# Optimization experiments

Hardware: AMD Instinct MI355X
Metric: run time of the kernel (lower is better)

The kernel has to match this reference:

```python
import jax, jax.numpy as jnp
import numpy as np
import math

V, P, D, L, H = 50257, 1024, 768, 12, 12
HD = D // H
DFF = 4 * D
B, S = 2, 1024
EPS = 1e-5


def setup_inputs() -> dict:
    key = jax.random.key(0)
    ks = jax.random.split(key, 8)
    sc = 0.02
    return {
        "input_ids": jax.random.randint(ks[0], (B, S), 0, V),
        "wte": jax.random.normal(ks[1], (V, D), jnp.float32) * sc,
        "wpe": jax.random.normal(ks[2], (P, D), jnp.float32) * sc,
        "ln1_g": jnp.ones((L, D), jnp.float32),
        "ln1_b": jnp.zeros((L, D), jnp.float32),
        "qkv_w": jax.random.normal(ks[3], (L, 3 * D, D), jnp.float32) * sc,
        "qkv_b": jnp.zeros((L, 3 * D), jnp.float32),
        "proj_w": jax.random.normal(ks[4], (L, D, D), jnp.float32) * sc,
        "proj_b": jnp.zeros((L, D), jnp.float32),
        "ln2_g": jnp.ones((L, D), jnp.float32),
        "ln2_b": jnp.zeros((L, D), jnp.float32),
        "fc_w": jax.random.normal(ks[5], (L, DFF, D), jnp.float32) * sc,
        "fc_b": jnp.zeros((L, DFF), jnp.float32),
        "cproj_w": jax.random.normal(ks[6], (L, D, DFF), jnp.float32) * sc,
        "cproj_b": jnp.zeros((L, D), jnp.float32),
        "lnf_g": jnp.ones((D,), jnp.float32),
        "lnf_b": jnp.zeros((D,), jnp.float32),
    }


def layer_norm(x, g, b):
    mu = jnp.mean(x, axis=-1, keepdims=True)
    var = jnp.mean(jnp.square(x - mu), axis=-1, keepdims=True)
    return (x - mu) * jax.lax.rsqrt(var + EPS) * g + b


def _forward(input_ids, wte, wpe, ln1_g, ln1_b, qkv_w, qkv_b, proj_w, proj_b,
             ln2_g, ln2_b, fc_w, fc_b, cproj_w, cproj_b, lnf_g, lnf_b):
    s = input_ids.shape[1]
    h = wte[input_ids] + wpe[jnp.arange(s)][None, :, :]  # [B,S,D]
    causal = jnp.tril(jnp.ones((s, s), bool))  # [S,S]
    neg_inf = jnp.finfo(h.dtype).min

    def step(x, p):
        l1g, l1b, qw, qb, pw, pb, l2g, l2b, fw, fb, cw, cb = p
        hn = layer_norm(x, l1g, l1b)
        qkv = hn @ qw.T + qb  # [B,S,3D]
        q, k, v = jnp.split(qkv, 3, axis=-1)
        q = q.reshape(B, s, H, HD).transpose(0, 2, 1, 3)  # [B,H,S,hd]
        k = k.reshape(B, s, H, HD).transpose(0, 2, 1, 3)
        v = v.reshape(B, s, H, HD).transpose(0, 2, 1, 3)
        scores = jnp.einsum("bhqd,bhkd->bhqk", q, k) / math.sqrt(HD)
        scores = jnp.where(causal[None, None], scores, neg_inf)
        attn = jax.nn.softmax(scores, axis=-1)
        o = jnp.einsum("bhqk,bhkd->bhqd", attn, v)
        o = o.transpose(0, 2, 1, 3).reshape(B, s, D)
        x = x + (o @ pw.T + pb)
        hn2 = layer_norm(x, l2g, l2b)
        m = jax.nn.gelu(hn2 @ fw.T + fb, approximate=False)
        x = x + (m @ cw.T + cb)
        return x, None

    params = (ln1_g, ln1_b, qkv_w, qkv_b, proj_w, proj_b,
              ln2_g, ln2_b, fc_w, fc_b, cproj_w, cproj_b)
    h, _ = jax.lax.scan(step, h, params)
    h = layer_norm(h, lnf_g, lnf_b)
    logits = h @ wte.T  # tied lm_head, [B,S,V]
    return logits


def reference(input_ids, wte, wpe, ln1_g, ln1_b, qkv_w, qkv_b, proj_w, proj_b,
              ln2_g, ln2_b, fc_w, fc_b, cproj_w, cproj_b, lnf_g, lnf_b):
    return _forward(input_ids, wte, wpe, ln1_g, ln1_b, qkv_w, qkv_b, proj_w,
                    proj_b, ln2_g, ln2_b, fc_w, fc_b, cproj_w, cproj_b,
                    lnf_g, lnf_b)
```

## Files before the change

kernel.cpp:

```cpp
#include <hip/hip_runtime.h>

#define BB 2
#define SS 1024
#define DM 768
#define NH 12
#define HDIM 64
#define NL 12
#define DFFN 3072
#define VOC 50257
#define ROWS (BB * SS)
#define MT (ROWS / 128)

typedef __attribute__((ext_vector_type(4))) float f32x4;
typedef __attribute__((ext_vector_type(8))) short short8;
typedef __attribute__((ext_vector_type(4))) short short4v;
typedef unsigned short ushort;

__device__ __forceinline__ ushort f2bf(float f) {
  union { float f; unsigned int u; } x; x.f = f;
  unsigned int u = x.u;
  unsigned int r = (u + 0x7FFFu + ((u >> 16) & 1u)) >> 16;
  return (ushort)r;
}

__global__ __launch_bounds__(256) void embed_k(const int* __restrict__ ids,
    const float* __restrict__ wte, const float* __restrict__ wpe,
    float* __restrict__ h) {
  const int row = blockIdx.x;
  const int s = row & (SS - 1);
  const int tid = threadIdx.x;
  const int id = ids[row];
  const size_t wbase = (size_t)id * DM;
  const size_t pbase = (size_t)s * DM;
  const size_t obase = (size_t)row * DM;
  h[obase + tid]       = wte[wbase + tid]       + wpe[pbase + tid];
  h[obase + tid + 256] = wte[wbase + tid + 256] + wpe[pbase + tid + 256];
  h[obase + tid + 512] = wte[wbase + tid + 512] + wpe[pbase + tid + 512];
}

__global__ __launch_bounds__(256) void f2b_k(const float* __restrict__ in,
                                             ushort* __restrict__ out, int n4) {
  for (int i = blockIdx.x * 256 + threadIdx.x; i < n4; i += gridDim.x * 256) {
    f32x4 v = ((const f32x4*)in)[i];
    short4v s;
    s[0] = f2bf(v[0]); s[1] = f2bf(v[1]); s[2] = f2bf(v[2]); s[3] = f2bf(v[3]);
    ((short4v*)out)[i] = s;
  }
}

template <int OB>
__global__ __launch_bounds__(256) void layernorm_t(const float* __restrict__ x,
    const float* __restrict__ g, const float* __restrict__ b, void* __restrict__ y) {
  const int tid = threadIdx.x;
  const int lane = tid & 63;
  const int wave = tid >> 6;
  const int row = blockIdx.x * 4 + wave;
  const size_t base = (size_t)row * DM;

  f32x4 v[3];
  float sum = 0.f;
#pragma unroll
  for (int k = 0; k < 3; k++) {
    v[k] = *(const f32x4*)&x[base + k * 256 + lane * 4];
    sum += v[k][0] + v[k][1] + v[k][2] + v[k][3];
  }
#pragma unroll
  for (int off = 32; off >= 1; off >>= 1) sum += __shfl_xor(sum, off);
  const float mu = sum * (1.0f / DM);

  float var = 0.f;
#pragma unroll
  for (int k = 0; k < 3; k++)
#pragma unroll
    for (int i = 0; i < 4; i++) {
      const float d = v[k][i] - mu;
      var += d * d;
    }
#pragma unroll
  for (int off = 32; off >= 1; off >>= 1) var += __shfl_xor(var, off);
  const float rstd = rsqrtf(var * (1.0f / DM) + 1e-5f);

#pragma unroll
  for (int k = 0; k < 3; k++) {
    const int col = k * 256 + lane * 4;
    f32x4 gv = *(const f32x4*)&g[col];
    f32x4 bv = *(const f32x4*)&b[col];
    if (OB) {
      short4v o;
#pragma unroll
      for (int i = 0; i < 4; i++)
        o[i] = f2bf((v[k][i] - mu) * rstd * gv[i] + bv[i]);
      *(short4v*)&((ushort*)y)[base + col] = o;
    } else {
      f32x4 o;
#pragma unroll
      for (int i = 0; i < 4; i++)
        o[i] = (v[k][i] - mu) * rstd * gv[i] + bv[i];
      *(f32x4*)&((float*)y)[base + col] = o;
    }
  }
}

template <int ROUNDS>
__device__ __forceinline__ void stage_sw(const ushort* __restrict__ g, int ldg,
                                         ushort* lds, int wave, int lane,
                                         int rowmax) {
#pragma unroll
  for (int r = 0; r < ROUNDS; r++) {
    const int chunk = (r * 4 + wave) * 64 + lane;
    const int nrow = chunk >> 3;
    const int cs = (chunk & 7) ^ (nrow & 7);
    const int row = nrow > rowmax ? rowmax : nrow;
    const ushort* ga = g + (size_t)row * ldg + cs * 8;
    ushort* la = lds + (r * 4 + wave) * 512;
    __builtin_amdgcn_global_load_lds(
        (const __attribute__((address_space(1))) unsigned int*)ga,
        (__attribute__((address_space(3))) unsigned int*)la, 16, 0, 0);
  }
}

__global__ __launch_bounds__(256) void gemm_lg(const ushort* __restrict__ A,
    const ushort* __restrict__ Bw, float* __restrict__ Cout, int N, int K) {
  __shared__ __align__(16) ushort smem[4 * 8192];
  ushort* AsL0 = smem;
  ushort* AsL1 = smem + 8192;
  ushort* BsL0 = smem + 16384;
  ushort* BsL1 = smem + 24576;

  const int tid = threadIdx.x;
  const int lane = tid & 63;
  const int wave = tid >> 6;
  const int la = lane & 15;
  const int hi = lane >> 4;
  const int swz = (la & 7) << 3;

  const int nwg = gridDim.x;
  int bid = blockIdx.x;
  {
    const int q = nwg >> 3, r = nwg & 7;
    const int xcd = bid & 7, idx = bid >> 3;
    bid = (xcd < r ? xcd * (q + 1) : r * (q + 1) + (xcd - r) * q) + idx;
  }
  const int m0 = (bid % MT) * 128;
  const int n0 = (bid / MT) * 128;

  const int wr = (wave >> 1) * 64;
  const int wc = (wave & 1) * 64;
  const int brmax = min(N - n0 - 1, 127);

  f32x4 acc[4][4];
#pragma unroll
  for (int i = 0; i < 4; i++)
#pragma unroll
    for (int j = 0; j < 4; j++) acc[i][j] = (f32x4){0.f, 0.f, 0.f, 0.f};

  const ushort* Ag = A + (size_t)m0 * K;
  const ushort* Bg = Bw + (size_t)n0 * K;

  const int nt = K >> 6;
  const int s0 = (bid % MT) % nt;

  stage_sw<4>(Ag + s0 * 64, K, AsL0, wave, lane, 127);
  stage_sw<4>(Bg + s0 * 64, K, BsL0, wave, lane, brmax);

  int cur = 0;
  for (int t = 0; t < nt; t++) {
    if (t + 1 < nt) {
      int sn = t + 1 + s0; if (sn >= nt) sn -= nt;
      stage_sw<4>(Ag + sn * 64, K, cur ? AsL0 : AsL1, wave, lane, 127);
      stage_sw<4>(Bg + sn * 64, K, cur ? BsL0 : BsL1, wave, lane, brmax);
      asm volatile("s_waitcnt vmcnt(8)" ::: "memory");
    } else {
      asm volatile("s_waitcnt vmcnt(0)" ::: "memory");
    }
    __builtin_amdgcn_s_barrier();
    __builtin_amdgcn_sched_barrier(0);

    const ushort* Ab = (cur ? AsL1 : AsL0) + (wr + la) * 64;
    const ushort* Bb = (cur ? BsL1 : BsL0) + (wc + la) * 64;
    __builtin_amdgcn_s_setprio(1);
#pragma unroll
    for (int ks = 0; ks < 2; ks++) {
      const int co = (ks * 32 + hi * 8) ^ swz;
      short8 a[4], b[4];
#pragma unroll
      for (int mi = 0; mi < 4; mi++)
        a[mi] = *(const short8*)(Ab + mi * 1024 + co);
#pragma unroll
      for (int ni = 0; ni < 4; ni++)
        b[ni] = *(const short8*)(Bb + ni * 1024 + co);
#pragma unroll
      for (int mi = 0; mi < 4; mi++)
#pragma unroll
        for (int ni = 0; ni < 4; ni++)
          acc[mi][ni] = __builtin_amdgcn_mfma_f32_16x16x32_bf16(
              a[mi], b[ni], acc[mi][ni], 0, 0, 0);
    }
    __builtin_amdgcn_s_setprio(0);
    __builtin_amdgcn_sched_barrier(0);
    __builtin_amdgcn_s_barrier();
    __builtin_amdgcn_sched_barrier(0);
    cur ^= 1;
  }

  float* L = (float*)smem;
  const int myhalf = wave & 1;
#pragma unroll
  for (int h = 0; h < 2; h++) {
    if (myhalf == h) {
#pragma unroll
      for (int mi = 0; mi < 4; mi++)
#pragma unroll
        for (int ni = 0; ni < 4; ni++)
#pragma unroll
          for (int j = 0; j < 4; j++) {
            const int row = wr + mi * 16 + 4 * hi + j;
            const int col = ni * 16 + la;
            L[row * 68 + col] = acc[mi][ni][j];
          }
    }
    __syncthreads();
#pragma unroll
    for (int it = 0; it < 32; it++) {
      const int flat = it * 256 + tid;
      const int row = flat >> 6, col = flat & 63;
      const int gc = n0 + h * 64 + col;
      if (gc < N)
        Cout[(size_t)(m0 + row) * N + gc] = L[row * 68 + col];
    }
    __syncthreads();
  }
}

template <int EPI, int OUTBF, int MR>
__global__ __launch_bounds__(256) void gemm_p3(const ushort* __restrict__ A,
    const ushort* __restrict__ Bw, const float* __restrict__ bias,
    const float* __restrict__ res, void* __restrict__ Cout, int N, int K) {
  constexpr int MROWS = MR * 32;
  constexpr int MTILES = ROWS / MROWS;
  constexpr int ASZ = MROWS * 64;
  constexpr int BSZ = 64 * 64;
  __shared__ __align__(16) ushort smem[3 * ASZ + 3 * BSZ];
  ushort* As = smem;
  ushort* Bs = smem + 3 * ASZ;

  const int tid = threadIdx.x;
  const int lane = tid & 63;
  const int wave = tid >> 6;
  const int la = lane & 15;
  const int hi = lane >> 4;
  const int swz = (la & 7) << 3;

  const int nwg = gridDim.x;
  int bid = blockIdx.x;
  {
    const int q = nwg >> 3, r = nwg & 7;
    const int xcd = bid & 7, idx = bid >> 3;
    bid = (xcd < r ? xcd * (q + 1) : r * (q + 1) + (xcd - r) * q) + idx;
  }
  const int m0 = (bid % MTILES) * MROWS;
  const int n0 = (bid / MTILES) * 64;

  const int wr = (wave >> 1) * (MROWS / 2);
  const int wc = (wave & 1) * 32;

  f32x4 acc[MR][2];
#pragma unroll
  for (int i = 0; i < MR; i++)
#pragma unroll
    for (int j = 0; j < 2; j++) acc[i][j] = (f32x4){0.f, 0.f, 0.f, 0.f};

  const ushort* Ag = A + (size_t)m0 * K;
  const ushort* Bg = Bw + (size_t)n0 * K;
  const int nt = K >> 6;
  const int s0 = (bid % MTILES) % nt;

  {
    int s1 = s0 + 1; if (s1 >= nt) s1 -= nt;
    stage_sw<MR>(Ag + s0 * 64, K, As, wave, lane, MROWS - 1);
    stage_sw<2>(Bg + s0 * 64, K, Bs, wave, lane, 63);
    stage_sw<MR>(Ag + s1 * 64, K, As + ASZ, wave, lane, MROWS - 1);
    stage_sw<2>(Bg + s1 * 64, K, Bs + BSZ, wave, lane, 63);
  }

  for (int t = 0; t < nt; t++) {
    if (t + 1 < nt) {
      asm volatile("s_waitcnt vmcnt(%0)" :: "i"(MR + 2) : "memory");
    } else {
      asm volatile("s_waitcnt vmcnt(0)" ::: "memory");
    }
    __builtin_amdgcn_s_barrier();
    __builtin_amdgcn_sched_barrier(0);

    const ushort* Ab = As + (t % 3) * ASZ + (wr + la) * 64;
    const ushort* Bb = Bs + (t % 3) * BSZ + (wc + la) * 64;
    __builtin_amdgcn_s_setprio(1);
#pragma unroll
    for (int ks = 0; ks < 2; ks++) {
      const int co = (ks * 32 + hi * 8) ^ swz;
      short8 a[MR], b[2];
#pragma unroll
      for (int mi = 0; mi < MR; mi++)
        a[mi] = *(const short8*)(Ab + mi * 1024 + co);
#pragma unroll
      for (int ni = 0; ni < 2; ni++)
        b[ni] = *(const short8*)(Bb + ni * 1024 + co);
#pragma unroll
      for (int mi = 0; mi < MR; mi++)
#pragma unroll
        for (int ni = 0; ni < 2; ni++)
          acc[mi][ni] = __builtin_amdgcn_mfma_f32_16x16x32_bf16(
              a[mi], b[ni], acc[mi][ni], 0, 0, 0);
    }
    __builtin_amdgcn_s_setprio(0);
    __builtin_amdgcn_sched_barrier(0);
    __builtin_amdgcn_s_barrier();
    __builtin_amdgcn_sched_barrier(0);
    if (t + 2 < nt) {
      int sn = t + 2 + s0; if (sn >= nt) sn -= nt;
      stage_sw<MR>(Ag + sn * 64, K, As + ((t + 2) % 3) * ASZ, wave, lane, MROWS - 1);
      stage_sw<2>(Bg + sn * 64, K, Bs + ((t + 2) % 3) * BSZ, wave, lane, 63);
    }
  }

  if (OUTBF) {
    ushort* L = smem;
#pragma unroll
    for (int mi = 0; mi < MR; mi++)
#pragma unroll
      for (int ni = 0; ni < 2; ni++)
#pragma unroll
        for (int j = 0; j < 4; j++) {
          const int row = wr + mi * 16 + 4 * hi + j;
          const int col = wc + ni * 16 + la;
          float x = acc[mi][ni][j];
          if (EPI >= 1) x += bias[n0 + col];
          if (EPI == 3) x = 0.5f * x * (1.0f + erff(x * 0.70710678118f));
          L[row * 72 + col] = f2bf(x);
        }
    __syncthreads();
    ushort* Co = (ushort*)Cout;
    constexpr int ITERS = MROWS * 64 / 8 / 256;
#pragma unroll
    for (int it = 0; it < ITERS; it++) {
      const int idx8 = it * 256 + tid;
      const int row = idx8 >> 3, c8 = idx8 & 7;
      short8 v = *(const short8*)&L[row * 72 + c8 * 8];
      *(short8*)&Co[(size_t)(m0 + row) * N + n0 + c8 * 8] = v;
    }
  } else {
    float* L = (float*)smem;
#pragma unroll
    for (int mi = 0; mi < MR; mi++)
#pragma unroll
      for (int ni = 0; ni < 2; ni++)
#pragma unroll
        for (int j = 0; j < 4; j++) {
          const int row = wr + mi * 16 + 4 * hi + j;
          const int col = wc + ni * 16 + la;
          float x = acc[mi][ni][j];
          if (EPI >= 1) x += bias[n0 + col];
          if (EPI == 3) x = 0.5f * x * (1.0f + erff(x * 0.70710678118f));
          L[row * 68 + col] = x;
        }
    __syncthreads();
    f32x4* Co = (f32x4*)Cout;
    const f32x4* R4 = (const f32x4*)res;
    constexpr int ITERS = MROWS * 64 / 4 / 256;
#pragma unroll
    for (int it = 0; it < ITERS; it++) {
      const int idx4 = it * 256 + tid;
      const int row = idx4 >> 4, c4 = idx4 & 15;
      f32x4 v = *(const f32x4*)&L[row * 68 + c4 * 4];
      const size_t o4 = ((size_t)(m0 + row) * N + n0) / 4 + c4;
      if (EPI == 2) v += R4[o4];
      Co[o4] = v;
    }
  }
}

__global__ __launch_bounds__(256) void attn_bf(const ushort* __restrict__ qkv,
                                               ushort* __restrict__ o) {
  const int tid = threadIdx.x;
  const int lane = tid & 63;
  const int wave = tid >> 6;
  const int hi = lane >> 4;
  const int la = lane & 15;
  const int q0 = blockIdx.x * 64;
  const int bh = blockIdx.y;
  const int bb = bh / NH;
  const int hh = bh % NH;
  const size_t rstride = 3 * DM;
  const ushort* base = qkv + (size_t)bb * SS * rstride;
  const ushort* kbase = base + DM + hh * HDIM;
  const ushort* vbase = base + 2 * DM + hh * HDIM;

  __shared__ ushort Ks[64][72];
  __shared__ ushort Vt[64][72];
  __shared__ ushort Pb[4][16][72];

  const int kr = tid >> 2;
  const int kc = (tid & 3) * 16;
  const int vp0 = (tid >> 3) * 2;
  const int vc = (tid & 7) * 8;

  short8 qf[2];
  {
    const int qrow = q0 + wave * 16 + la;
    const ushort* qp = base + (size_t)qrow * rstride + hh * HDIM + 8 * hi;
    qf[0] = *(const short8*)qp;
    qf[1] = *(const short8*)(qp + 32);
  }

  short8 kA, kB, vA, vB;
  {
    const ushort* kp = kbase + (size_t)kr * rstride + kc;
    kA = *(const short8*)kp;
    kB = *(const short8*)(kp + 8);
    const ushort* vp = vbase + (size_t)vp0 * rstride + vc;
    vA = *(const short8*)vp;
    vB = *(const short8*)(vp + rstride);
  }

  f32x4 accO[4] = {};
  float m_[4], l_[4];
#pragma unroll
  for (int j = 0; j < 4; j++) { m_[j] = -1e30f; l_[j] = 0.f; }

  const int nt = q0 / 64 + 1;
  for (int kt = 0; kt < nt; kt++) {
    __syncthreads();
    *(short8*)&Ks[kr][kc]     = kA;
    *(short8*)&Ks[kr][kc + 8] = kB;
#pragma unroll
    for (int i = 0; i < 8; i++) {
      unsigned int pk = (unsigned int)(unsigned short)vA[i] |
                        ((unsigned int)(unsigned short)vB[i] << 16);
      *(unsigned int*)&Vt[vc + i][vp0] = pk;
    }
    __syncthreads();
    if (kt + 1 < nt) {
      const ushort* kp = kbase + (size_t)((kt + 1) * 64 + kr) * rstride + kc;
      kA = *(const short8*)kp;
      kB = *(const short8*)(kp + 8);
      const ushort* vp = vbase + (size_t)((kt + 1) * 64 + vp0) * rstride + vc;
      vA = *(const short8*)vp;
      vB = *(const short8*)(vp + rstride);
    }

    f32x4 s[4] = {};
#pragma unroll
    for (int f = 0; f < 4; f++) {
#pragma unroll
      for (int kk = 0; kk < 2; kk++) {
        short8 kf = *(const short8*)&Ks[f * 16 + la][kk * 32 + 8 * hi];
        s[f] = __builtin_amdgcn_mfma_f32_16x16x32_bf16(qf[kk], kf, s[f], 0, 0, 0);
      }
#pragma unroll
      for (int j = 0; j < 4; j++) s[f][j] *= 0.125f;
    }

    if (kt == nt - 1) {
      const int qr = wave * 16 + 4 * hi;
#pragma unroll
      for (int f = 0; f < 4; f++) {
        const int kcol = f * 16 + la;
#pragma unroll
        for (int j = 0; j < 4; j++)
          if (kcol > qr + j) s[f][j] = -1e30f;
      }
    }

#pragma unroll
    for (int j = 0; j < 4; j++) {
      float rm = fmaxf(fmaxf(s[0][j], s[1][j]), fmaxf(s[2][j], s[3][j]));
      rm = fmaxf(rm, __shfl_xor(rm, 1));
      rm = fmaxf(rm, __shfl_xor(rm, 2));
      rm = fmaxf(rm, __shfl_xor(rm, 4));
      rm = fmaxf(rm, __shfl_xor(rm, 8));
      const float mnew = fmaxf(m_[j], rm);
      const float alpha = expf(m_[j] - mnew);
      float rs = 0.f;
#pragma unroll
      for (int f = 0; f < 4; f++) {
        const float p = expf(s[f][j] - mnew);
        s[f][j] = p;
        rs += p;
      }
      rs += __shfl_xor(rs, 1);
      rs += __shfl_xor(rs, 2);
      rs += __shfl_xor(rs, 4);
      rs += __shfl_xor(rs, 8);
      l_[j] = l_[j] * alpha + rs;
      m_[j] = mnew;
#pragma unroll
      for (int f = 0; f < 4; f++) accO[f][j] *= alpha;
    }

#pragma unroll
    for (int f = 0; f < 4; f++)
#pragma unroll
      for (int j = 0; j < 4; j++)
        Pb[wave][4 * hi + j][f * 16 + la] = f2bf(s[f][j]);

    short8 pf0 = *(const short8*)&Pb[wave][la][8 * hi];
    short8 pf1 = *(const short8*)&Pb[wave][la][32 + 8 * hi];
#pragma unroll
    for (int f = 0; f < 4; f++) {
      short8 vf0 = *(const short8*)&Vt[f * 16 + la][8 * hi];
      short8 vf1 = *(const short8*)&Vt[f * 16 + la][32 + 8 * hi];
      accO[f] = __builtin_amdgcn_mfma_f32_16x16x32_bf16(pf0, vf0, accO[f], 0, 0, 0);
      accO[f] = __builtin_amdgcn_mfma_f32_16x16x32_bf16(pf1, vf1, accO[f], 0, 0, 0);
    }
  }

  ushort* op = o + (size_t)(bb * SS + q0 + wave * 16) * DM + hh * HDIM;
#pragma unroll
  for (int j = 0; j < 4; j++) {
    const float inv = 1.0f / l_[j];
    const int qr = 4 * hi + j;
#pragma unroll
    for (int f = 0; f < 4; f++)
      op[(size_t)qr * DM + f * 16 + la] = f2bf(accO[f][j] * inv);
  }
}

template <int EPI>
__global__ __launch_bounds__(256) void gemm_nt(const float* __restrict__ A,
    const float* __restrict__ Bw, const float* __restrict__ bias,
    const float* __restrict__ res, float* __restrict__ C, int N, int K) {
  __shared__ ushort As[64][40];
  __shared__ ushort Bs[64][40];
  const int tid = threadIdx.x;
  const int m0 = blockIdx.y * 64;
  const int n0 = blockIdx.x * 64;
  const int lane = tid & 63;
  const int wave = tid >> 6;
  const int wr = (wave >> 1) * 32;
  const int wc = (wave & 1) * 32;
  const int lr = lane & 15;
  const int lk = (lane >> 4) * 8;
  const int sr = tid >> 2;
  const int sc = (tid & 3) * 8;
  f32x4 acc[2][2] = {};
  for (int kk = 0; kk < K; kk += 32) {
    {
      const float* p = A + (size_t)(m0 + sr) * K + kk + sc;
      f32x4 v0 = *(const f32x4*)p;
      f32x4 v1 = *(const f32x4*)(p + 4);
      short8 sv;
      for (int i = 0; i < 4; i++) { sv[i] = f2bf(v0[i]); sv[4 + i] = f2bf(v1[i]); }
      *(short8*)&As[sr][sc] = sv;
    }
    {
      const int gr = n0 + sr;
      short8 sv = {};
      if (gr < N) {
        const float* p = Bw + (size_t)gr * K + kk + sc;
        f32x4 v0 = *(const f32x4*)p;
        f32x4 v1 = *(const f32x4*)(p + 4);
        for (int i = 0; i < 4; i++) { sv[i] = f2bf(v0[i]); sv[4 + i] = f2bf(v1[i]); }
      }
      *(short8*)&Bs[sr][sc] = sv;
    }
    __syncthreads();
    short8 a0 = *(const short8*)&As[wr + lr][lk];
    short8 a1 = *(const short8*)&As[wr + 16 + lr][lk];
    short8 b0 = *(const short8*)&Bs[wc + lr][lk];
    short8 b1 = *(const short8*)&Bs[wc + 16 + lr][lk];
    acc[0][0] = __builtin_amdgcn_mfma_f32_16x16x32_bf16(a0, b0, acc[0][0], 0, 0, 0);
    acc[0][1] = __builtin_amdgcn_mfma_f32_16x16x32_bf16(a0, b1, acc[0][1], 0, 0, 0);
    acc[1][0] = __builtin_amdgcn_mfma_f32_16x16x32_bf16(a1, b0, acc[1][0], 0, 0, 0);
    acc[1][1] = __builtin_amdgcn_mfma_f32_16x16x32_bf16(a1, b1, acc[1][1], 0, 0, 0);
    __syncthreads();
  }
  const int orow = (lane >> 4) * 4;
  for (int mi = 0; mi < 2; mi++)
    for (int ni = 0; ni < 2; ni++) {
      const int col = n0 + wc + ni * 16 + lr;
      if (col >= N) continue;
      for (int j = 0; j < 4; j++) {
        const int row = m0 + wr + mi * 16 + orow + j;
        float x = acc[mi][ni][j];
        if (EPI >= 1) x += bias[col];
        const size_t idx = (size_t)row * N + col;
        if (EPI == 2) x += res[idx];
        if (EPI == 3) x = 0.5f * x * (1.0f + erff(x * 0.70710678118f));
        C[idx] = x;
      }
    }
}

__global__ __launch_bounds__(256) void attn_f32(const float* __restrict__ qkv,
                                                float* __restrict__ o) {
  const int tid = threadIdx.x;
  const int lane = tid & 63;
  const int wave = tid >> 6;
  const int hi = lane >> 4;
  const int la = lane & 15;
  const int q0 = blockIdx.x * 64;
  const int bh = blockIdx.y;
  const int bb = bh / NH;
  const int hh = bh % NH;
  const size_t rstride = 3 * DM;
  const float* base = qkv + (size_t)bb * SS * rstride;
  __shared__ ushort Ks[64][72];
  __shared__ ushort Vt[64][72];
  __shared__ ushort Pb[4][16][72];
  short8 qf[2];
  {
    const int qrow = q0 + wave * 16 + la;
    const float* qp = base + (size_t)qrow * rstride + hh * HDIM + 8 * hi;
    for (int kk = 0; kk < 2; kk++) {
      f32x4 v0 = *(const f32x4*)(qp + 32 * kk);
      f32x4 v1 = *(const f32x4*)(qp + 32 * kk + 4);
      short8 sv;
      for (int i = 0; i < 4; i++) {
        sv[i] = f2bf(v0[i] * 0.125f); sv[4 + i] = f2bf(v1[i] * 0.125f);
      }
      qf[kk] = sv;
    }
  }
  f32x4 accO[4] = {};
  float m_[4], l_[4];
  for (int j = 0; j < 4; j++) { m_[j] = -1e30f; l_[j] = 0.f; }
  const int nt = q0 / 64 + 1;
  for (int kt = 0; kt < nt; kt++) {
    __syncthreads();
    {
      const int r = tid >> 2;
      const int c = (tid & 3) * 16;
      const float* kp = base + (size_t)(kt * 64 + r) * rstride + DM + hh * HDIM + c;
      const float* vp = kp + DM;
      f32x4 k0 = *(const f32x4*)kp, k1 = *(const f32x4*)(kp + 4);
      f32x4 k2 = *(const f32x4*)(kp + 8), k3 = *(const f32x4*)(kp + 12);
      short8 s0, s1;
      for (int i = 0; i < 4; i++) {
        s0[i] = f2bf(k0[i]); s0[4 + i] = f2bf(k1[i]);
        s1[i] = f2bf(k2[i]); s1[4 + i] = f2bf(k3[i]);
      }
      *(short8*)&Ks[r][c] = s0;
      *(short8*)&Ks[r][c + 8] = s1;
      f32x4 v0 = *(const f32x4*)vp, v1 = *(const f32x4*)(vp + 4);
      f32x4 v2 = *(const f32x4*)(vp + 8), v3 = *(const f32x4*)(vp + 12);
      for (int i = 0; i < 4; i++) {
        Vt[c + i][r] = f2bf(v0[i]); Vt[c + 4 + i][r] = f2bf(v1[i]);
        Vt[c + 8 + i][r] = f2bf(v2[i]); Vt[c + 12 + i][r] = f2bf(v3[i]);
      }
    }
    __syncthreads();
    f32x4 s[4] = {};
    for (int f = 0; f < 4; f++)
      for (int kk = 0; kk < 2; kk++) {
        short8 kf = *(const short8*)&Ks[f * 16 + la][kk * 32 + 8 * hi];
        s[f] = __builtin_amdgcn_mfma_f32_16x16x32_bf16(qf[kk], kf, s[f], 0, 0, 0);
      }
    if (kt == nt - 1) {
      const int qr = wave * 16 + 4 * hi;
      for (int f = 0; f < 4; f++) {
        const int kcol = f * 16 + la;
        for (int j = 0; j < 4; j++)
          if (kcol > qr + j) s[f][j] = -1e30f;
      }
    }
    for (int j = 0; j < 4; j++) {
      float rm = fmaxf(fmaxf(s[0][j], s[1][j]), fmaxf(s[2][j], s[3][j]));
      rm = fmaxf(rm, __shfl_xor(rm, 1));
      rm = fmaxf(rm, __shfl_xor(rm, 2));
      rm = fmaxf(rm, __shfl_xor(rm, 4));
      rm = fmaxf(rm, __shfl_xor(rm, 8));
      const float mnew = fmaxf(m_[j], rm);
      const float alpha = expf(m_[j] - mnew);
      float rs = 0.f;
      for (int f = 0; f < 4; f++) {
        const float p = expf(s[f][j] - mnew);
        s[f][j] = p; rs += p;
      }
      rs += __shfl_xor(rs, 1);
      rs += __shfl_xor(rs, 2);
      rs += __shfl_xor(rs, 4);
      rs += __shfl_xor(rs, 8);
      l_[j] = l_[j] * alpha + rs;
      m_[j] = mnew;
      for (int f = 0; f < 4; f++) accO[f][j] *= alpha;
    }
    for (int f = 0; f < 4; f++)
      for (int j = 0; j < 4; j++)
        Pb[wave][4 * hi + j][f * 16 + la] = f2bf(s[f][j]);
    short8 pf0 = *(const short8*)&Pb[wave][la][8 * hi];
    short8 pf1 = *(const short8*)&Pb[wave][la][32 + 8 * hi];
    for (int f = 0; f < 4; f++) {
      short8 vf0 = *(const short8*)&Vt[f * 16 + la][8 * hi];
      short8 vf1 = *(const short8*)&Vt[f * 16 + la][32 + 8 * hi];
      accO[f] = __builtin_amdgcn_mfma_f32_16x16x32_bf16(pf0, vf0, accO[f], 0, 0, 0);
      accO[f] = __builtin_amdgcn_mfma_f32_16x16x32_bf16(pf1, vf1, accO[f], 0, 0, 0);
    }
  }
  float* op = o + (size_t)(bb * SS + q0 + wave * 16) * DM + hh * HDIM;
  for (int j = 0; j < 4; j++) {
    const float inv = 1.0f / l_[j];
    const int qr = 4 * hi + j;
    for (int f = 0; f < 4; f++)
      op[(size_t)qr * DM + f * 16 + la] = accO[f][j] * inv;
  }
}

extern "C" void kernel_launch(void* const* d_in, const int* in_sizes, int n_in,
                              void* d_out, int out_size, void* d_ws,
                              size_t ws_size, hipStream_t stream) {
  const int*   ids     = (const int*)d_in[0];
  const float* wte     = (const float*)d_in[1];
  const float* wpe     = (const float*)d_in[2];
  const float* ln1_g   = (const float*)d_in[3];
  const float* ln1_b   = (const float*)d_in[4];
  const float* qkv_w   = (const float*)d_in[5];
  const float* qkv_b   = (const float*)d_in[6];
  const float* proj_w  = (const float*)d_in[7];
  const float* proj_b  = (const float*)d_in[8];
  const float* ln2_g   = (const float*)d_in[9];
  const float* ln2_b   = (const float*)d_in[10];
  const float* fc_w    = (const float*)d_in[11];
  const float* fc_b    = (const float*)d_in[12];
  const float* cproj_w = (const float*)d_in[13];
  const float* cproj_b = (const float*)d_in[14];
  const float* lnf_g   = (const float*)d_in[15];
  const float* lnf_b   = (const float*)d_in[16];
  float* out = (float*)d_out;

  const size_t sz_h    = (size_t)ROWS * DM * 4;
  const size_t sz_hn   = (size_t)ROWS * DM * 2;
  const size_t sz_qkv  = (size_t)ROWS * 3 * DM * 2;
  const size_t sz_ob   = (size_t)ROWS * DM * 2;
  const size_t sz_mb   = (size_t)ROWS * DFFN * 2;
  const size_t sz_wq   = (size_t)NL * 3 * DM * DM * 2;
  const size_t sz_wp   = (size_t)NL * DM * DM * 2;
  const size_t sz_wf   = (size_t)NL * DFFN * DM * 2;
  const size_t sz_wc   = (size_t)NL * DM * DFFN * 2;
  const size_t sz_wt   = (size_t)VOC * DM * 2;
  const size_t NEED = sz_h + sz_hn + sz_qkv + sz_ob + sz_mb +
                      sz_wq + sz_wp + sz_wf + sz_wc + sz_wt;

  if (ws_size >= NEED) {
    char* p = (char*)d_ws;
    float*  h    = (float*)p;  p += sz_h;
    ushort* hn   = (ushort*)p; p += sz_hn;
    ushort* qkvb = (ushort*)p; p += sz_qkv;
    ushort* ob   = (ushort*)p; p += sz_ob;
    ushort* mb   = (ushort*)p; p += sz_mb;
    ushort* wq   = (ushort*)p; p += sz_wq;
    ushort* wp   = (ushort*)p; p += sz_wp;
    ushort* wf   = (ushort*)p; p += sz_wf;
    ushort* wc   = (ushort*)p; p += sz_wc;
    ushort* wt   = (ushort*)p; p += sz_wt;

    f2b_k<<<2048, 256, 0, stream>>>(qkv_w,   wq, NL * 3 * DM * DM / 4);
    f2b_k<<<1024, 256, 0, stream>>>(proj_w,  wp, NL * DM * DM / 4);
    f2b_k<<<2048, 256, 0, stream>>>(fc_w,    wf, NL * DFFN * DM / 4);
    f2b_k<<<2048, 256, 0, stream>>>(cproj_w, wc, NL * DM * DFFN / 4);
    f2b_k<<<2048, 256, 0, stream>>>(wte,     wt, VOC * DM / 4);

    embed_k<<<ROWS, 256, 0, stream>>>(ids, wte, wpe, h);

    for (int l = 0; l < NL; l++) {
      layernorm_t<1><<<ROWS / 4, 256, 0, stream>>>(h, ln1_g + l * DM, ln1_b + l * DM, hn);
      gemm_p3<1, 1, 4><<<MT * (3 * DM / 64), 256, 0, stream>>>(
          hn, wq + (size_t)l * 3 * DM * DM, qkv_b + (size_t)l * 3 * DM,
          nullptr, qkvb, 3 * DM, DM);
      attn_bf<<<dim3(SS / 64, BB * NH), 256, 0, stream>>>(qkvb, ob);
      gemm_p3<2, 0, 2><<<(ROWS / 64) * (DM / 64), 256, 0, stream>>>(
          ob, wp + (size_t)l * DM * DM, proj_b + (size_t)l * DM, h, h, DM, DM);
      layernorm_t<1><<<ROWS / 4, 256, 0, stream>>>(h, ln2_g + l * DM, ln2_b + l * DM, hn);
      gemm_p3<3, 1, 4><<<MT * (DFFN / 64), 256, 0, stream>>>(
          hn, wf + (size_t)l * DFFN * DM, fc_b + (size_t)l * DFFN,
          nullptr, mb, DFFN, DM);
      gemm_p3<2, 0, 2><<<(ROWS / 64) * (DM / 64), 256, 0, stream>>>(
          mb, wc + (size_t)l * DM * DFFN, cproj_b + (size_t)l * DM, h, h,
          DM, DFFN);
    }

    layernorm_t<1><<<ROWS / 4, 256, 0, stream>>>(h, lnf_g, lnf_b, hn);
    gemm_lg<<<MT * ((VOC + 127) / 128), 256, 0, stream>>>(
        hn, wt, out, VOC, DM);
  } else {
    float* ws = (float*)d_ws;
    float* h   = ws;
    float* hn  = h + (size_t)ROWS * DM;
    float* qkv = hn + (size_t)ROWS * DM;
    float* ob  = qkv + (size_t)ROWS * 3 * DM;
    float* mb  = ob + (size_t)ROWS * DM;

    embed_k<<<ROWS, 256, 0, stream>>>(ids, wte, wpe, h);
    for (int l = 0; l < NL; l++) {
      layernorm_t<0><<<ROWS / 4, 256, 0, stream>>>(h, ln1_g + l * DM, ln1_b + l * DM, hn);
      gemm_nt<1><<<dim3(3 * DM / 64, ROWS / 64), 256, 0, stream>>>(
          hn, qkv_w + (size_t)l * 3 * DM * DM, qkv_b + (size_t)l * 3 * DM,
          nullptr, qkv, 3 * DM, DM);
      attn_f32<<<dim3(SS / 64, BB * NH), 256, 0, stream>>>(qkv, ob);
      gemm_nt<2><<<dim3(DM / 64, ROWS / 64), 256, 0, stream>>>(
          ob, proj_w + (size_t)l * DM * DM, proj_b + (size_t)l * DM, h, h, DM, DM);
      layernorm_t<0><<<ROWS / 4, 256, 0, stream>>>(h, ln2_g + l * DM, ln2_b + l * DM, hn);
      gemm_nt<3><<<dim3(DFFN / 64, ROWS / 64), 256, 0, stream>>>(
          hn, fc_w + (size_t)l * DFFN * DM, fc_b + (size_t)l * DFFN,
          nullptr, mb, DFFN, DM);
      gemm_nt<2><<<dim3(DM / 64, ROWS / 64), 256, 0, stream>>>(
          mb, cproj_w + (size_t)l * DM * DFFN, cproj_b + (size_t)l * DM, h, h,
          DM, DFFN);
    }
    layernorm_t<0><<<ROWS / 4, 256, 0, stream>>>(h, lnf_g, lnf_b, hn);
    gemm_nt<0><<<dim3((VOC + 63) / 64, ROWS / 64), 256, 0, stream>>>(
        hn, wte, nullptr, nullptr, out, VOC, DM);
  }
}
```

Measured before the change: 2.015 ms.

## Use 256x256 tiles with 512 threads for the LM-head GEMM, add attention setprio

Replaces the 128x128, 256-thread LM-head GEMM with a 256x256 tile kernel using 8 waves. Each wave computes 128x64 and the K-step is split into four sub-phases, with next-tile global-to-LDS loads issued during the first two. The larger tile raises arithmetic intensity and reduces how often A and B are reloaded across the large vocab dimension. The cost is more LDS per block (64KB), more registers and more barriers, plus wasted work on the ragged final N tile. Attention MFMA sections are also wrapped in s_setprio to favour matrix issue.

```diff
diff --git a/kernel.cpp b/kernel.cpp
--- a/kernel.cpp
+++ b/kernel.cpp
@@ -119,20 +119,39 @@
   }
 }
 
-__global__ __launch_bounds__(256) void gemm_lg(const ushort* __restrict__ A,
+__device__ __forceinline__ void stage_half(const ushort* __restrict__ g, int ldg,
+                                           ushort* lds, int rbase, int rowmax,
+                                           int tid) {
+#pragma unroll
+  for (int i = 0; i < 2; i++) {
+    const int c = i * 512 + tid;
+    const int nrow = c >> 3;
+    const int cs = (c & 7) ^ (nrow & 7);
+    int row = rbase + nrow;
+    if (row > rowmax) row = rowmax;
+    const ushort* ga = g + (size_t)row * ldg + cs * 8;
+    ushort* la = lds + (size_t)(i * 512 + (tid & ~63)) * 8;
+    __builtin_amdgcn_global_load_lds(
+        (const __attribute__((address_space(1))) unsigned int*)ga,
+        (__attribute__((address_space(3))) unsigned int*)la, 16, 0, 0);
+  }
+}
+
+__global__ __launch_bounds__(512, 2) void gemm_256(const ushort* __restrict__ A,
     const ushort* __restrict__ Bw, float* __restrict__ Cout, int N, int K) {
-  __shared__ __align__(16) ushort smem[4 * 8192];
-  ushort* AsL0 = smem;
-  ushort* AsL1 = smem + 8192;
-  ushort* BsL0 = smem + 16384;
-  ushort* BsL1 = smem + 24576;
+  constexpr int TSZ = 256 * 64;
+  __shared__ __align__(16) ushort smem[4 * TSZ];
+  ushort* As = smem;
+  ushort* Bs = smem + 2 * TSZ;
 
   const int tid = threadIdx.x;
   const int lane = tid & 63;
-  const int wave = tid >> 6;
   const int la = lane & 15;
   const int hi = lane >> 4;
   const int swz = (la & 7) << 3;
+  const int wave = tid >> 6;
+  const int wr2 = wave >> 2;
+  const int wc2 = wave & 3;
 
   const int nwg = gridDim.x;
   int bid = blockIdx.x;
@@ -141,80 +160,96 @@
     const int xcd = bid & 7, idx = bid >> 3;
     bid = (xcd < r ? xcd * (q + 1) : r * (q + 1) + (xcd - r) * q) + idx;
   }
-  const int m0 = (bid % MT) * 128;
-  const int n0 = (bid / MT) * 128;
-
-  const int wr = (wave >> 1) * 64;
-  const int wc = (wave & 1) * 64;
-  const int brmax = min(N - n0 - 1, 127);
-
-  f32x4 acc[4][4];
-#pragma unroll
-  for (int i = 0; i < 4; i++)
+  const int m0 = (bid & 7) * 256;
+  const int n0 = (bid >> 3) * 256;
+  const int brmax = min(N - n0 - 1, 255);
+
+  f32x4 acc[8][4];
+#pragma unroll
+  for (int i = 0; i < 8; i++)
 #pragma unroll
     for (int j = 0; j < 4; j++) acc[i][j] = (f32x4){0.f, 0.f, 0.f, 0.f};
 
   const ushort* Ag = A + (size_t)m0 * K;
   const ushort* Bg = Bw + (size_t)n0 * K;
-
   const int nt = K >> 6;
-  const int s0 = (bid % MT) % nt;
-
-  stage_sw<4>(Ag + s0 * 64, K, AsL0, wave, lane, 127);
-  stage_sw<4>(Bg + s0 * 64, K, BsL0, wave, lane, brmax);
-
-  int cur = 0;
+  const int s0 = bid % nt;
+
+  {
+    const ushort* Ags = Ag + s0 * 64;
+    const ushort* Bgs = Bg + s0 * 64;
+    stage_half(Ags, K, As, 0, 255, tid);
+    stage_half(Ags, K, As + 8192, 128, 255, tid);
+    stage_half(Bgs, K, Bs, 0, brmax, tid);
+    stage_half(Bgs, K, Bs + 8192, 128, brmax, tid);
+  }
+  asm volatile("s_waitcnt vmcnt(0)" ::: "memory");
+  __builtin_amdgcn_s_barrier();
+  __builtin_amdgcn_sched_barrier(0);
+
   for (int t = 0; t < nt; t++) {
+    const int cb = t & 1, nb = cb ^ 1;
+    const ushort* Abase = As + cb * TSZ + (wr2 * 128 + la) * 64;
+    const ushort* Bbase = Bs + cb * TSZ + (wc2 * 64 + la) * 64;
+
+#pragma unroll
+    for (int q = 0; q < 4; q++) {
+      if (t + 1 < nt) {
+        int sn = t + 1 + s0; if (sn >= nt) sn -= nt;
+        if (q == 0) {
+          stage_half(Ag + sn * 64, K, As + nb * TSZ, 0, 255, tid);
+          stage_half(Ag + sn * 64, K, As + nb * TSZ + 8192, 128, 255, tid);
+        } else if (q == 1) {
+          stage_half(Bg + sn * 64, K, Bs + nb * TSZ, 0, brmax, tid);
+          stage_half(Bg + sn * 64, K, Bs + nb * TSZ + 8192, 128, brmax, tid);
+        }
+      }
+      const int mq = q >> 1, nq = q & 1;
+      short8 a[2][4], b[2][2];
+#pragma unroll
+      for (int ks = 0; ks < 2; ks++) {
+        const int co = (ks * 32 + hi * 8) ^ swz;
+#pragma unroll
+        for (int i = 0; i < 4; i++)
+          a[ks][i] = *(const short8*)(Abase + (mq * 64 + i * 16) * 64 + co);
+#pragma unroll
+        for (int j = 0; j < 2; j++)
+          b[ks][j] = *(const short8*)(Bbase + (nq * 32 + j * 16) * 64 + co);
+      }
+      __builtin_amdgcn_s_barrier();
+      asm volatile("s_waitcnt lgkmcnt(0)" ::: "memory");
+      __builtin_amdgcn_sched_barrier(0);
+      __builtin_amdgcn_s_setprio(1);
+#pragma unroll
+      for (int ks = 0; ks < 2; ks++)
+#pragma unroll
+        for (int i = 0; i < 4; i++)
+#pragma unroll
+          for (int j = 0; j < 2; j++)
+            acc[mq * 4 + i][nq * 2 + j] = __builtin_amdgcn_mfma_f32_16x16x32_bf16(
+                a[ks][i], b[ks][j], acc[mq * 4 + i][nq * 2 + j], 0, 0, 0);
+      __builtin_amdgcn_s_setprio(0);
+      __builtin_amdgcn_sched_barrier(0);
+      __builtin_amdgcn_s_barrier();
+    }
     if (t + 1 < nt) {
-      int sn = t + 1 + s0; if (sn >= nt) sn -= nt;
-      stage_sw<4>(Ag + sn * 64, K, cur ? AsL0 : AsL1, wave, lane, 127);
-      stage_sw<4>(Bg + sn * 64, K, cur ? BsL0 : BsL1, wave, lane, brmax);
-      asm volatile("s_waitcnt vmcnt(8)" ::: "memory");
-    } else {
       asm volatile("s_waitcnt vmcnt(0)" ::: "memory");
-    }
-    __builtin_amdgcn_s_barrier();
-    __builtin_amdgcn_sched_barrier(0);
-
-    const ushort* Ab = (cur ? AsL1 : AsL0) + (wr + la) * 64;
-    const ushort* Bb = (cur ? BsL1 : BsL0) + (wc + la) * 64;
-    __builtin_amdgcn_s_setprio(1);
-#pragma unroll
-    for (int ks = 0; ks < 2; ks++) {
-      const int co = (ks * 32 + hi * 8) ^ swz;
-      short8 a[4], b[4];
-#pragma unroll
-      for (int mi = 0; mi < 4; mi++)
-        a[mi] = *(const short8*)(Ab + mi * 1024 + co);
-#pragma unroll
-      for (int ni = 0; ni < 4; ni++)
-        b[ni] = *(const short8*)(Bb + ni * 1024 + co);
-#pragma unroll
-      for (int mi = 0; mi < 4; mi++)
+      __builtin_amdgcn_s_barrier();
+      __builtin_amdgcn_sched_barrier(0);
+    }
+  }
+
+  float* L = (float*)smem;
+#pragma unroll
+  for (int p = 0; p < 4; p++) {
+    if (wc2 == p) {
+#pragma unroll
+      for (int mi = 0; mi < 8; mi++)
 #pragma unroll
         for (int ni = 0; ni < 4; ni++)
-          acc[mi][ni] = __builtin_amdgcn_mfma_f32_16x16x32_bf16(
-              a[mi], b[ni], acc[mi][ni], 0, 0, 0);
-    }
-    __builtin_amdgcn_s_setprio(0);
-    __builtin_amdgcn_sched_barrier(0);
-    __builtin_amdgcn_s_barrier();
-    __builtin_amdgcn_sched_barrier(0);
-    cur ^= 1;
-  }
-
-  float* L = (float*)smem;
-  const int myhalf = wave & 1;
-#pragma unroll
-  for (int h = 0; h < 2; h++) {
-    if (myhalf == h) {
-#pragma unroll
-      for (int mi = 0; mi < 4; mi++)
-#pragma unroll
-        for (int ni = 0; ni < 4; ni++)
 #pragma unroll
           for (int j = 0; j < 4; j++) {
-            const int row = wr + mi * 16 + 4 * hi + j;
+            const int row = wr2 * 128 + mi * 16 + 4 * hi + j;
             const int col = ni * 16 + la;
             L[row * 68 + col] = acc[mi][ni][j];
           }
@@ -222,9 +257,9 @@
     __syncthreads();
 #pragma unroll
     for (int it = 0; it < 32; it++) {
-      const int flat = it * 256 + tid;
+      const int flat = it * 512 + tid;
       const int row = flat >> 6, col = flat & 63;
-      const int gc = n0 + h * 64 + col;
+      const int gc = n0 + p * 64 + col;
       if (gc < N)
         Cout[(size_t)(m0 + row) * N + gc] = L[row * 68 + col];
     }
@@ -449,6 +484,7 @@
     }
 
     f32x4 s[4] = {};
+    __builtin_amdgcn_s_setprio(1);
 #pragma unroll
     for (int f = 0; f < 4; f++) {
 #pragma unroll
@@ -456,9 +492,12 @@
         short8 kf = *(const short8*)&Ks[f * 16 + la][kk * 32 + 8 * hi];
         s[f] = __builtin_amdgcn_mfma_f32_16x16x32_bf16(qf[kk], kf, s[f], 0, 0, 0);
       }
+    }
+    __builtin_amdgcn_s_setprio(0);
+#pragma unroll
+    for (int f = 0; f < 4; f++)
 #pragma unroll
       for (int j = 0; j < 4; j++) s[f][j] *= 0.125f;
-    }
 
     if (kt == nt - 1) {
       const int qr = wave * 16 + 4 * hi;
@@ -505,6 +544,7 @@
 
     short8 pf0 = *(const short8*)&Pb[wave][la][8 * hi];
     short8 pf1 = *(const short8*)&Pb[wave][la][32 + 8 * hi];
+    __builtin_amdgcn_s_setprio(1);
 #pragma unroll
     for (int f = 0; f < 4; f++) {
       short8 vf0 = *(const short8*)&Vt[f * 16 + la][8 * hi];
@@ -512,6 +552,7 @@
       accO[f] = __builtin_amdgcn_mfma_f32_16x16x32_bf16(pf0, vf0, accO[f], 0, 0, 0);
       accO[f] = __builtin_amdgcn_mfma_f32_16x16x32_bf16(pf1, vf1, accO[f], 0, 0, 0);
     }
+    __builtin_amdgcn_s_setprio(0);
   }
 
   ushort* op = o + (size_t)(bb * SS + q0 + wave * 16) * DM + hh * HDIM;
@@ -779,7 +820,7 @@
     }
 
     layernorm_t<1><<<ROWS / 4, 256, 0, stream>>>(h, lnf_g, lnf_b, hn);
-    gemm_lg<<<MT * ((VOC + 127) / 128), 256, 0, stream>>>(
+    gemm_256<<<8 * ((VOC + 255) / 256), 512, 0, stream>>>(
         hn, wt, out, VOC, DM);
   } else {
     float* ws = (float*)d_ws;
```

Result: slower. 2.072 ms (+2.8%).
